# Performance work log

Hardware: AMD Instinct MI355X
Metric: run time of the kernel (lower is better)

Reference implementation:

```python
import jax, jax.numpy as jnp
import numpy as np

N_ACTIVE = 1_000_000
GRID = 256          # detector voxel grid per axis
C_IN = 32
C_OUT = 32
K = 27              # 3x3x3 submanifold filter taps
BN_EPS = 1e-4       # scn.BatchNormReLU default eps


def _build_neighbor_idx(rng):
    """Sample unique active voxels in a GRID^3 volume and build the 27-tap
    rulebook: neighbor_idx[i, k] = row of the active voxel at offset k from
    voxel i, or -1 if that site is inactive / out of bounds."""
    lin = np.sort(rng.choice(GRID ** 3, size=N_ACTIVE, replace=False))  # sorted linear coords
    z = lin // (GRID * GRID)
    y = (lin // GRID) % GRID
    x = lin % GRID
    offs = np.array([(dz, dy, dx) for dz in (-1, 0, 1) for dy in (-1, 0, 1) for dx in (-1, 0, 1)],
                    dtype=np.int64)  # [27, 3]
    nz = z[:, None] + offs[None, :, 0]
    ny = y[:, None] + offs[None, :, 1]
    nx = x[:, None] + offs[None, :, 2]
    inb = (nz >= 0) & (nz < GRID) & (ny >= 0) & (ny < GRID) & (nx >= 0) & (nx < GRID)
    nlin = (nz * GRID + ny) * GRID + nx
    pos = np.searchsorted(lin, nlin)
    pos_c = np.clip(pos, 0, N_ACTIVE - 1)
    found = inb & (lin[pos_c] == nlin)
    return np.where(found, pos_c, -1).astype(np.int32)  # [N, 27]


def setup_inputs() -> dict:
    key = jax.random.key(0)
    k1, k2 = jax.random.split(key)
    rng = np.random.default_rng(0)
    neighbor_idx = jnp.asarray(_build_neighbor_idx(rng))
    features = jax.random.normal(k1, (N_ACTIVE, C_IN), dtype=jnp.float32)
    w_scale = 1.0 / np.sqrt(K * C_IN)
    weight = jax.random.normal(k2, (K, C_IN, C_OUT), dtype=jnp.float32) * w_scale
    gamma = jnp.ones((C_OUT,), dtype=jnp.float32)
    beta = jnp.zeros((C_OUT,), dtype=jnp.float32)
    return {"features": features, "weight": weight, "gamma": gamma,
            "beta": beta, "neighbor_idx": neighbor_idx}


def reference(features, weight, gamma, beta, neighbor_idx):
    # Submanifold sparse conv: output defined only at the N active sites.
    n = features.shape[0]
    mask = neighbor_idx >= 0                       # [N, 27]
    safe_idx = jnp.where(mask, neighbor_idx, 0)    # [N, 27]
    out = jnp.zeros((n, weight.shape[2]), dtype=features.dtype)
    for k in range(K):  # fixed structural loop over 27 filter taps
        gathered = features[safe_idx[:, k]] * mask[:, k][:, None]  # [N, Cin]
        out = out + gathered @ weight[k]                            # [N, Cout]
    # Fused BatchNorm (training-mode stats over active voxels) + ReLU
    mean = jnp.mean(out, axis=0)
    var = jnp.mean(jnp.square(out - mean), axis=0)  # biased var, as in BN
    out = (out - mean) * jax.lax.rsqrt(var + BN_EPS) * gamma + beta
    return jnp.maximum(out, 0.0)
```

## Files before the change

### kernel.cpp

```cpp
#include <hip/hip_runtime.h>
#include <hip/hip_bf16.h>

#define C_CH 32
#define K_TAPS 27
#define CONV_GRID 2048

typedef short bf16x8 __attribute__((ext_vector_type(8)));
typedef float f32x4 __attribute__((ext_vector_type(4)));

__global__ __launch_bounds__(256) void convert_weights_kernel(
    const float* __restrict__ wt, short* __restrict__ wbf)
{
    int t = blockIdx.x * 256 + threadIdx.x;
    if (t < K_TAPS * 1024) {
        int e = t & 7, l = (t >> 3) & 63, half = (t >> 9) & 1, k = t >> 10;
        int ci = (l >> 4) * 8 + e;
        int j  = half * 16 + (l & 15);
        union { __hip_bfloat16 h; short s; } u;
        u.h = __float2bfloat16(wt[k * 1024 + ci * 32 + j]);
        wbf[t] = u.s;
    }
}

__global__ __launch_bounds__(256) void conv_mfma_kernel(
    const float* __restrict__ feat,
    const short* __restrict__ wbf,
    const int*   __restrict__ nbr,
    float* __restrict__ out,
    float* __restrict__ stats,
    int n)
{
    __shared__ float bsum[C_CH];
    __shared__ float bsq[C_CH];
    const int tid = threadIdx.x;
    if (tid < C_CH) { bsum[tid] = 0.0f; bsq[tid] = 0.0f; }
    __syncthreads();

    const int l   = tid & 63;
    const int wv  = tid >> 6;
    const int row = l & 15;
    const int kq  = l >> 4;
    const int n_batches   = (n + 15) >> 4;
    const int wave_gid    = blockIdx.x * 4 + wv;
    const int total_waves = gridDim.x * 4;

    float ps0 = 0.0f, ps1 = 0.0f, pq0 = 0.0f, pq1 = 0.0f;

    for (int b = wave_gid; b < n_batches; b += total_waves) {
        const int vbase = b << 4;
        const int myv   = vbase + row;
        const bool rowok = myv < n;

        int idxs[K_TAPS];
        #pragma unroll
        for (int k = 0; k < K_TAPS; ++k)
            idxs[k] = rowok ? nbr[(size_t)myv * K_TAPS + k] : -1;

        f32x4 acc0 = {0.f, 0.f, 0.f, 0.f};
        f32x4 acc1 = {0.f, 0.f, 0.f, 0.f};

        #pragma unroll
        for (int k = 0; k < K_TAPS; ++k) {
            const int idx = idxs[k];
            const bool valid = idx >= 0;
            if (__ballot(valid) == 0) continue;

            bf16x8 a = {0, 0, 0, 0, 0, 0, 0, 0};
            if (valid) {
                const float4* fp =
                    (const float4*)(feat + (size_t)idx * C_CH + kq * 8);
                float4 f0 = fp[0];
                float4 f1 = fp[1];
                union { bf16x8 v; __hip_bfloat162 h[4]; } au;
                au.h[0] = __float22bfloat162_rn(make_float2(f0.x, f0.y));
                au.h[1] = __float22bfloat162_rn(make_float2(f0.z, f0.w));
                au.h[2] = __float22bfloat162_rn(make_float2(f1.x, f1.y));
                au.h[3] = __float22bfloat162_rn(make_float2(f1.z, f1.w));
                a = au.v;
            }

            bf16x8 b0 = *(const bf16x8*)(wbf + (((k * 2 + 0) * 64 + l) << 3));
            bf16x8 b1 = *(const bf16x8*)(wbf + (((k * 2 + 1) * 64 + l) << 3));

            acc0 = __builtin_amdgcn_mfma_f32_16x16x32_bf16(a, b0, acc0, 0, 0, 0);
            acc1 = __builtin_amdgcn_mfma_f32_16x16x32_bf16(a, b1, acc1, 0, 0, 0);
        }

        #pragma unroll
        for (int r = 0; r < 4; ++r) {
            const int orow = vbase + kq * 4 + r;
            if (orow < n) {
                const float v0 = acc0[r];
                const float v1 = acc1[r];
                out[(size_t)orow * C_CH + (l & 15)]      = v0;
                out[(size_t)orow * C_CH + 16 + (l & 15)] = v1;
                ps0 += v0; pq0 += v0 * v0;
                ps1 += v1; pq1 += v1 * v1;
            }
        }
    }

    ps0 += __shfl_xor(ps0, 16); ps0 += __shfl_xor(ps0, 32);
    ps1 += __shfl_xor(ps1, 16); ps1 += __shfl_xor(ps1, 32);
    pq0 += __shfl_xor(pq0, 16); pq0 += __shfl_xor(pq0, 32);
    pq1 += __shfl_xor(pq1, 16); pq1 += __shfl_xor(pq1, 32);

    if (l < 16) {
        atomicAdd(&bsum[l],      ps0);
        atomicAdd(&bsum[16 + l], ps1);
        atomicAdd(&bsq[l],       pq0);
        atomicAdd(&bsq[16 + l],  pq1);
    }
    __syncthreads();
    if (tid < C_CH) {
        atomicAdd(&stats[tid],        bsum[tid]);
        atomicAdd(&stats[C_CH + tid], bsq[tid]);
    }
}

__global__ void bn_finalize_kernel(const float* __restrict__ stats,
                                   float* __restrict__ ss,
                                   const float* __restrict__ gamma,
                                   const float* __restrict__ beta,
                                   float inv_n)
{
    int j = threadIdx.x;
    if (j < C_CH) {
        float mean = stats[j] * inv_n;
        float var  = stats[C_CH + j] * inv_n - mean * mean;
        float sc   = gamma[j] * rsqrtf(var + 1e-4f);
        ss[j]        = sc;
        ss[C_CH + j] = beta[j] - mean * sc;
    }
}

__global__ __launch_bounds__(256) void bn_apply_kernel(
    float* __restrict__ out, const float* __restrict__ ss, int total4)
{
    int e = blockIdx.x * blockDim.x + threadIdx.x;
    if (e < total4) {
        float4 v = ((float4*)out)[e];
        int c4 = e & 7;
        float4 sc = ((const float4*)ss)[c4];
        float4 sh = ((const float4*)(ss + C_CH))[c4];
        v.x = fmaxf(fmaf(v.x, sc.x, sh.x), 0.0f);
        v.y = fmaxf(fmaf(v.y, sc.y, sh.y), 0.0f);
        v.z = fmaxf(fmaf(v.z, sc.z, sh.z), 0.0f);
        v.w = fmaxf(fmaf(v.w, sc.w, sh.w), 0.0f);
        ((float4*)out)[e] = v;
    }
}

extern "C" void kernel_launch(void* const* d_in, const int* in_sizes, int n_in,
                              void* d_out, int out_size, void* d_ws, size_t ws_size,
                              hipStream_t stream) {
    const float* feat  = (const float*)d_in[0];
    const float* wt    = (const float*)d_in[1];
    const float* gamma = (const float*)d_in[2];
    const float* beta  = (const float*)d_in[3];
    const int*   nbr   = (const int*)d_in[4];

    float* out   = (float*)d_out;
    float* stats = (float*)d_ws;
    float* ss    = stats + 2 * C_CH;
    short* wbf   = (short*)(ss + 2 * C_CH);

    const int n = in_sizes[0] / C_CH;

    hipMemsetAsync(stats, 0, 2 * C_CH * sizeof(float), stream);

    convert_weights_kernel<<<(K_TAPS * 1024 + 255) / 256, 256, 0, stream>>>(wt, wbf);

    conv_mfma_kernel<<<CONV_GRID, 256, 0, stream>>>(feat, wbf, nbr, out, stats, n);

    bn_finalize_kernel<<<1, 64, 0, stream>>>(stats, ss, gamma, beta,
                                             1.0f / (float)n);

    const int total4 = n * C_CH / 4;
    bn_apply_kernel<<<(total4 + 255) / 256, 256, 0, stream>>>(out, ss, total4);
}
```

Baseline: 712.2 us.

## Grow conv grid, gather branchlessly, fold BN finalize into apply kernel

Raises the conv grid from 2048 to 8192 blocks, so each wave handles fewer 16-row batches and more waves are in flight to hide gather latency. The per-tap ballot skip and divergent load are replaced by an unconditional load from a clamped index followed by a select, which removes branches but gathers row 0 for missing neighbours. The one-block BN finalize kernel is folded into the apply kernel, where each block recomputes scale and shift into shared memory, saving one launch.

```diff
diff --git a/kernel.cpp b/kernel.cpp
--- a/kernel.cpp
+++ b/kernel.cpp
@@ -3,7 +3,7 @@
 
 #define C_CH 32
 #define K_TAPS 27
-#define CONV_GRID 2048
+#define CONV_GRID 8192
 
 typedef short bf16x8 __attribute__((ext_vector_type(8)));
 typedef float f32x4 __attribute__((ext_vector_type(4)));
@@ -42,7 +42,7 @@
     const int kq  = l >> 4;
     const int n_batches   = (n + 15) >> 4;
     const int wave_gid    = blockIdx.x * 4 + wv;
-    const int total_waves = gridDim.x * 4;
+    const int total_waves = CONV_GRID * 4;
 
     float ps0 = 0.0f, ps1 = 0.0f, pq0 = 0.0f, pq1 = 0.0f;
 
@@ -61,23 +61,22 @@
 
         #pragma unroll
         for (int k = 0; k < K_TAPS; ++k) {
-            const int idx = idxs[k];
+            const int  idx   = idxs[k];
             const bool valid = idx >= 0;
-            if (__ballot(valid) == 0) continue;
+            const int  safe  = valid ? idx : 0;
 
-            bf16x8 a = {0, 0, 0, 0, 0, 0, 0, 0};
-            if (valid) {
-                const float4* fp =
-                    (const float4*)(feat + (size_t)idx * C_CH + kq * 8);
-                float4 f0 = fp[0];
-                float4 f1 = fp[1];
-                union { bf16x8 v; __hip_bfloat162 h[4]; } au;
-                au.h[0] = __float22bfloat162_rn(make_float2(f0.x, f0.y));
-                au.h[1] = __float22bfloat162_rn(make_float2(f0.z, f0.w));
-                au.h[2] = __float22bfloat162_rn(make_float2(f1.x, f1.y));
-                au.h[3] = __float22bfloat162_rn(make_float2(f1.z, f1.w));
-                a = au.v;
-            }
+            const float4* fp =
+                (const float4*)(feat + (size_t)safe * C_CH + kq * 8);
+            float4 f0 = fp[0];
+            float4 f1 = fp[1];
+
+            union { bf16x8 v; __hip_bfloat162 h[4]; } au;
+            au.h[0] = __float22bfloat162_rn(make_float2(f0.x, f0.y));
+            au.h[1] = __float22bfloat162_rn(make_float2(f0.z, f0.w));
+            au.h[2] = __float22bfloat162_rn(make_float2(f1.x, f1.y));
+            au.h[3] = __float22bfloat162_rn(make_float2(f1.z, f1.w));
+            const bf16x8 zero = {0, 0, 0, 0, 0, 0, 0, 0};
+            bf16x8 a = valid ? au.v : zero;
 
             bf16x8 b0 = *(const bf16x8*)(wbf + (((k * 2 + 0) * 64 + l) << 3));
             bf16x8 b1 = *(const bf16x8*)(wbf + (((k * 2 + 1) * 64 + l) << 3));
@@ -118,35 +117,33 @@
     }
 }
 
-__global__ void bn_finalize_kernel(const float* __restrict__ stats,
-                                   float* __restrict__ ss,
-                                   const float* __restrict__ gamma,
-                                   const float* __restrict__ beta,
-                                   float inv_n)
+__global__ __launch_bounds__(256) void bn_apply_kernel(
+    float* __restrict__ out,
+    const float* __restrict__ stats,
+    const float* __restrict__ gamma,
+    const float* __restrict__ beta,
+    float inv_n, int total4)
 {
-    int j = threadIdx.x;
-    if (j < C_CH) {
+    __shared__ float s_sc[C_CH];
+    __shared__ float s_sh[C_CH];
+    if (threadIdx.x < C_CH) {
+        int j = threadIdx.x;
         float mean = stats[j] * inv_n;
         float var  = stats[C_CH + j] * inv_n - mean * mean;
         float sc   = gamma[j] * rsqrtf(var + 1e-4f);
-        ss[j]        = sc;
-        ss[C_CH + j] = beta[j] - mean * sc;
+        s_sc[j] = sc;
+        s_sh[j] = beta[j] - mean * sc;
     }
-}
+    __syncthreads();
 
-__global__ __launch_bounds__(256) void bn_apply_kernel(
-    float* __restrict__ out, const float* __restrict__ ss, int total4)
-{
-    int e = blockIdx.x * blockDim.x + threadIdx.x;
+    int e = blockIdx.x * 256 + threadIdx.x;
     if (e < total4) {
         float4 v = ((float4*)out)[e];
-        int c4 = e & 7;
-        float4 sc = ((const float4*)ss)[c4];
-        float4 sh = ((const float4*)(ss + C_CH))[c4];
-        v.x = fmaxf(fmaf(v.x, sc.x, sh.x), 0.0f);
-        v.y = fmaxf(fmaf(v.y, sc.y, sh.y), 0.0f);
-        v.z = fmaxf(fmaf(v.z, sc.z, sh.z), 0.0f);
-        v.w = fmaxf(fmaf(v.w, sc.w, sh.w), 0.0f);
+        int c = (e & 7) * 4;
+        v.x = fmaxf(fmaf(v.x, s_sc[c + 0], s_sh[c + 0]), 0.0f);
+        v.y = fmaxf(fmaf(v.y, s_sc[c + 1], s_sh[c + 1]), 0.0f);
+        v.z = fmaxf(fmaf(v.z, s_sc[c + 2], s_sh[c + 2]), 0.0f);
+        v.w = fmaxf(fmaf(v.w, s_sc[c + 3], s_sh[c + 3]), 0.0f);
         ((float4*)out)[e] = v;
     }
 }
@@ -162,8 +159,7 @@
 
     float* out   = (float*)d_out;
     float* stats = (float*)d_ws;
-    float* ss    = stats + 2 * C_CH;
-    short* wbf   = (short*)(ss + 2 * C_CH);
+    short* wbf   = (short*)(stats + 2 * C_CH);
 
     const int n = in_sizes[0] / C_CH;
 
@@ -173,9 +169,7 @@
 
     conv_mfma_kernel<<<CONV_GRID, 256, 0, stream>>>(feat, wbf, nbr, out, stats, n);
 
-    bn_finalize_kernel<<<1, 64, 0, stream>>>(stats, ss, gamma, beta,
-                                             1.0f / (float)n);
-
     const int total4 = n * C_CH / 4;
-    bn_apply_kernel<<<(total4 + 255) / 256, 256, 0, stream>>>(out, ss, total4);
+    bn_apply_kernel<<<(total4 + 255) / 256, 256, 0, stream>>>(
+        out, stats, gamma, beta, 1.0f / (float)n, total4);
 }
```

New measurement: 1.027 ms. 44.2% more time.
